# Kernel optimization log

Hardware: AMD Instinct MI355X
Metric: run time of the kernel (lower is better)

## Reference

```python
import jax, jax.numpy as jnp
import numpy as np

IN_F = 4096
OUT_F = 11008
GROUP = 128
NGROUPS = IN_F // GROUP
MAX_INT = 15  # 2**4 - 1


def setup_inputs() -> dict:
    key = jax.random.key(0)
    k1, k2, k3, k4, k5 = jax.random.split(key, 5)
    x = jax.random.normal(k1, (4, 2048, IN_F), dtype=jnp.float32)
    qweight = jax.random.randint(k2, (OUT_F, IN_F), 0, MAX_INT + 1, dtype=jnp.int32)
    scales = jax.random.uniform(k3, (OUT_F, NGROUPS), dtype=jnp.float32) * 0.01 + 1e-4
    zeros = jax.random.uniform(k4, (OUT_F, NGROUPS), dtype=jnp.float32) * MAX_INT
    b = jax.random.normal(k5, (OUT_F,), dtype=jnp.float32)
    return {"x": x, "qweight": qweight, "scales": scales, "zeros": zeros, "b": b}


def reference(x, qweight, scales, zeros, b):
    # Group-wise dequantization: W[o, i] = (q[o, i] - zeros[o, g(i)]) * scales[o, g(i)]
    s_rep = jnp.repeat(scales, GROUP, axis=1)  # [OUT_F, IN_F]
    z_rep = jnp.repeat(zeros, GROUP, axis=1)   # [OUT_F, IN_F]
    w_fp = (qweight.astype(x.dtype) - z_rep.astype(x.dtype)) * s_rep.astype(x.dtype)
    # F.linear: x @ W.T + b
    out = jnp.einsum('bsi,oi->bso', x, w_fp) + b.astype(x.dtype)
    return out
```

## Files before the change

### kernel.cpp

```cpp
#include <hip/hip_runtime.h>
#include <hip/hip_bf16.h>


#define K_DIM 4096
#define N_DIM 11008
#define M_DIM 8192
#define NGRP 32

typedef __bf16 bf16x8 __attribute__((ext_vector_type(8)));
typedef float f32x4 __attribute__((ext_vector_type(4)));
typedef unsigned short u16x8 __attribute__((ext_vector_type(8)));

__device__ __forceinline__ unsigned short f2bf(float f) {
  unsigned u = __builtin_bit_cast(unsigned, f);
  return (unsigned short)((u + 0x7FFFu + ((u >> 16) & 1u)) >> 16);
}

__device__ __forceinline__ void gload_lds16(const void* g, void* l) {
  __builtin_amdgcn_global_load_lds(
      (const __attribute__((address_space(1))) unsigned int*)(unsigned long long)g,
      (__attribute__((address_space(3))) unsigned int*)(unsigned int)(unsigned long long)l,
      16, 0, 0);
}

__global__ __launch_bounds__(256) void cvt_x_kernel(const float4* __restrict__ x4,
                                                    u16x8* __restrict__ xb) {
  int i = blockIdx.x * 256 + threadIdx.x;
  float4 a = x4[2 * i], b = x4[2 * i + 1];
  u16x8 r;
  r[0] = f2bf(a.x); r[1] = f2bf(a.y); r[2] = f2bf(a.z); r[3] = f2bf(a.w);
  r[4] = f2bf(b.x); r[5] = f2bf(b.y); r[6] = f2bf(b.z); r[7] = f2bf(b.w);
  xb[i] = r;
}

__global__ __launch_bounds__(256) void dequant_kernel(const int4* __restrict__ q4,
                                                      const float* __restrict__ scales,
                                                      const float* __restrict__ zeros,
                                                      u16x8* __restrict__ wb) {
  int t = blockIdx.x * 256 + threadIdx.x;
  int o = t >> 9;
  int j8 = t & 511;
  int g = j8 >> 4;
  float s = scales[o * NGRP + g];
  float z = zeros[o * NGRP + g];
  float nzs = -z * s;
  int4 qa = q4[2 * t], qb = q4[2 * t + 1];
  u16x8 r;
  r[0] = f2bf(fmaf((float)qa.x, s, nzs));
  r[1] = f2bf(fmaf((float)qa.y, s, nzs));
  r[2] = f2bf(fmaf((float)qa.z, s, nzs));
  r[3] = f2bf(fmaf((float)qa.w, s, nzs));
  r[4] = f2bf(fmaf((float)qb.x, s, nzs));
  r[5] = f2bf(fmaf((float)qb.y, s, nzs));
  r[6] = f2bf(fmaf((float)qb.z, s, nzs));
  r[7] = f2bf(fmaf((float)qb.w, s, nzs));
  wb[t] = r;
}

#define BAR() __builtin_amdgcn_s_barrier()
#define SCHED0() __builtin_amdgcn_sched_barrier(0)

__global__ __launch_bounds__(512, 2) void gemm_kernel(const unsigned short* __restrict__ A,
                                                      const unsigned short* __restrict__ B,
                                                      const float* __restrict__ bias,
                                                      float* __restrict__ C) {
  extern __shared__ unsigned short smem[];
  unsigned short* sAb = smem;
  unsigned short* sBb = smem + 32768;

  const int bid = blockIdx.x;
  const int swz = (bid & 7) * 172 + (bid >> 3);
  const int tm = swz / 43, tn = swz % 43;

  const int tid = threadIdx.x;
  const int w = tid >> 6, l = tid & 63;
  const int wr = w >> 2, wc = w & 3;

  const int dsto = w * 512 + l * 8;
  const int gs = (l & 7) ^ (l >> 3);
  const unsigned short* gA = A + (size_t)(tm * 256 + (tid >> 3)) * K_DIM + gs * 8;
  const unsigned short* gB = B + (size_t)(tn * 256 + (tid >> 3)) * K_DIM + gs * 8;

#define STG_A(tt, h, dst)                                                       \
  do {                                                                          \
    const unsigned short* _s = gA + (size_t)(h) * 128 * K_DIM + (tt) * 64;      \
    gload_lds16(_s, (dst) + dsto);                                              \
    gload_lds16(_s + 64 * K_DIM, (dst) + 4096 + dsto);                          \
  } while (0)
#define STG_B(tt, h, dst)                                                       \
  do {                                                                          \
    const unsigned short* _s = gB + (size_t)(h) * 128 * K_DIM + (tt) * 64;      \
    gload_lds16(_s, (dst) + dsto);                                              \
    gload_lds16(_s + 64 * K_DIM, (dst) + 4096 + dsto);                          \
  } while (0)

  const int fr = l & 15, sb = l >> 4, x7 = l & 7;
  const int abase = (wr * 64 + fr) * 64;
  const int bbase = (wc * 32 + fr) * 64;
  const int k0 = (sb ^ x7) * 8;
  const int k1 = ((sb + 4) ^ x7) * 8;

  bf16x8 av[4][2], bva[2][2], bvb[2][2];
  f32x4 acc[8][4] = {};

#define READ_A(half)                                                     \
  {                                                                      \
    _Pragma("unroll") for (int m = 0; m < 4; ++m) {                      \
      av[m][0] = *(const bf16x8*)((half) + abase + m * 1024 + k0);       \
      av[m][1] = *(const bf16x8*)((half) + abase + m * 1024 + k1);       \
    }                                                                    \
  }
#define READ_B(half, arr)                                                \
  {                                                                      \
    _Pragma("unroll") for (int n = 0; n < 2; ++n) {                      \
      arr[n][0] = *(const bf16x8*)((half) + bbase + n * 1024 + k0);      \
      arr[n][1] = *(const bf16x8*)((half) + bbase + n * 1024 + k1);      \
    }                                                                    \
  }
#define MFMA_Q(mh, nh, arr)                                                        \
  {                                                                                \
    __builtin_amdgcn_s_setprio(1);                                                 \
    _Pragma("unroll") for (int kk = 0; kk < 2; ++kk)                               \
    _Pragma("unroll") for (int m = 0; m < 4; ++m)                                  \
    _Pragma("unroll") for (int nn = 0; nn < 2; ++nn)                               \
      acc[(mh)*4 + m][(nh)*2 + nn] = __builtin_amdgcn_mfma_f32_16x16x32_bf16(      \
          av[m][kk], arr[nn][kk], acc[(mh)*4 + m][(nh)*2 + nn], 0, 0, 0);          \
    __builtin_amdgcn_s_setprio(0);                                                 \
  }

#define TILE(tnext, curA, curB, nxtA, nxtB, has_next)                    \
  {                                                                      \
    if (has_next) {                                                      \
      STG_A(tnext, 0, nxtA);                                             \
      STG_A(tnext, 1, (nxtA) + 8192);                                    \
      STG_B(tnext, 0, nxtB);                                             \
      STG_B(tnext, 1, (nxtB) + 8192);                                    \
    }                                                                    \
    READ_A(curA);                                                        \
    READ_B(curB, bva);                                                   \
    READ_B((curB) + 8192, bvb);                                          \
    MFMA_Q(0, 0, bva);                                                   \
    MFMA_Q(0, 1, bvb);                                                   \
    READ_A((curA) + 8192);                                               \
    MFMA_Q(1, 1, bvb);                                                   \
    MFMA_Q(1, 0, bva);                                                   \
    asm volatile("s_waitcnt vmcnt(0)" ::: "memory");                     \
    BAR();                                                               \
    SCHED0();                                                            \
  }

  STG_A(0, 0, sAb);
  STG_A(0, 1, sAb + 8192);
  STG_B(0, 0, sBb);
  STG_B(0, 1, sBb + 8192);
  asm volatile("s_waitcnt vmcnt(0)" ::: "memory");
  BAR();
  SCHED0();

  for (int tt = 0; tt < 32; ++tt) {
    TILE(2 * tt + 1, sAb, sBb, sAb + 16384, sBb + 16384, 1);
    TILE(2 * tt + 2, sAb + 16384, sBb + 16384, sAb, sBb, (tt < 31));
  }

  const int r0 = tm * 256 + wr * 64 + sb * 4;
  const int c0 = tn * 256 + wc * 32 + fr;
#pragma unroll
  for (int n = 0; n < 4; ++n) {
    const int col = c0 + (n >> 1) * 128 + (n & 1) * 16;
    const float bv = bias[col];
#pragma unroll
    for (int mi = 0; mi < 8; ++mi) {
      const int row = r0 + (mi >> 2) * 128 + (mi & 3) * 16;
#pragma unroll
      for (int jj = 0; jj < 4; ++jj)
        C[(size_t)(row + jj) * N_DIM + col] = acc[mi][n][jj] + bv;
    }
  }
}

extern "C" void kernel_launch(void* const* d_in, const int* in_sizes, int n_in,
                              void* d_out, int out_size, void* d_ws, size_t ws_size,
                              hipStream_t stream) {
  const float* x = (const float*)d_in[0];
  const int* qw = (const int*)d_in[1];
  const float* sc = (const float*)d_in[2];
  const float* zr = (const float*)d_in[3];
  const float* bs = (const float*)d_in[4];
  float* out = (float*)d_out;

  const size_t xb_bytes = (size_t)M_DIM * K_DIM * 2;
  const size_t wb_bytes = (size_t)N_DIM * K_DIM * 2;
  if (ws_size < xb_bytes + wb_bytes) return;

  unsigned short* xb = (unsigned short*)d_ws;
  unsigned short* wb = (unsigned short*)((char*)d_ws + xb_bytes);

  (void)hipFuncSetAttribute((const void*)gemm_kernel,
                            hipFuncAttributeMaxDynamicSharedMemorySize, 131072);

  cvt_x_kernel<<<(M_DIM * K_DIM / 8) / 256, 256, 0, stream>>>((const float4*)x, (u16x8*)xb);
  dequant_kernel<<<(N_DIM * K_DIM / 8) / 256, 256, 0, stream>>>((const int4*)qw, sc, zr,
                                                                (u16x8*)wb);
  gemm_kernel<<<(M_DIM / 256) * (N_DIM / 256), 512, 131072, stream>>>(xb, wb, bs, out);
}
```

Baseline: 751.6 us.

## Restructure GEMM LDS pipeline to read-then-stage and merge the prep kernels

The GEMM main loop now reads the whole A and B tiles from LDS into registers up front, using a second A register set. It then waits and synchronises, issues the global-to-LDS loads for tile t+2 into the buffer it just freed, and runs all MFMAs under raised priority. The prologue preloads two tiles, so global loads overlap a full tile of compute instead of being issued before the reads. The x conversion and weight dequant kernels are merged into one launch to drop a kernel boundary. In exchange, register pressure goes up, and the per-tile vmcnt(0) wait plus barrier still serialises part of the pipeline.

Measured after the change: 865.2 us. 1.15x slower.

```diff
diff --git a/kernel.cpp b/kernel.cpp
--- a/kernel.cpp
+++ b/kernel.cpp
@@ -23,38 +23,40 @@
       16, 0, 0);
 }
 
-__global__ __launch_bounds__(256) void cvt_x_kernel(const float4* __restrict__ x4,
-                                                    u16x8* __restrict__ xb) {
-  int i = blockIdx.x * 256 + threadIdx.x;
-  float4 a = x4[2 * i], b = x4[2 * i + 1];
-  u16x8 r;
-  r[0] = f2bf(a.x); r[1] = f2bf(a.y); r[2] = f2bf(a.z); r[3] = f2bf(a.w);
-  r[4] = f2bf(b.x); r[5] = f2bf(b.y); r[6] = f2bf(b.z); r[7] = f2bf(b.w);
-  xb[i] = r;
-}
-
-__global__ __launch_bounds__(256) void dequant_kernel(const int4* __restrict__ q4,
-                                                      const float* __restrict__ scales,
-                                                      const float* __restrict__ zeros,
-                                                      u16x8* __restrict__ wb) {
-  int t = blockIdx.x * 256 + threadIdx.x;
-  int o = t >> 9;
-  int j8 = t & 511;
-  int g = j8 >> 4;
-  float s = scales[o * NGRP + g];
-  float z = zeros[o * NGRP + g];
-  float nzs = -z * s;
-  int4 qa = q4[2 * t], qb = q4[2 * t + 1];
-  u16x8 r;
-  r[0] = f2bf(fmaf((float)qa.x, s, nzs));
-  r[1] = f2bf(fmaf((float)qa.y, s, nzs));
-  r[2] = f2bf(fmaf((float)qa.z, s, nzs));
-  r[3] = f2bf(fmaf((float)qa.w, s, nzs));
-  r[4] = f2bf(fmaf((float)qb.x, s, nzs));
-  r[5] = f2bf(fmaf((float)qb.y, s, nzs));
-  r[6] = f2bf(fmaf((float)qb.z, s, nzs));
-  r[7] = f2bf(fmaf((float)qb.w, s, nzs));
-  wb[t] = r;
+__global__ __launch_bounds__(256) void prep_kernel(const float4* __restrict__ x4,
+                                                   const int4* __restrict__ q4,
+                                                   const float* __restrict__ scales,
+                                                   const float* __restrict__ zeros,
+                                                   u16x8* __restrict__ xb,
+                                                   u16x8* __restrict__ wb) {
+  const int bid = blockIdx.x;
+  if (bid < 16384) {
+    int i = bid * 256 + threadIdx.x;
+    float4 a = x4[2 * i], b = x4[2 * i + 1];
+    u16x8 r;
+    r[0] = f2bf(a.x); r[1] = f2bf(a.y); r[2] = f2bf(a.z); r[3] = f2bf(a.w);
+    r[4] = f2bf(b.x); r[5] = f2bf(b.y); r[6] = f2bf(b.z); r[7] = f2bf(b.w);
+    xb[i] = r;
+  } else {
+    int t = (bid - 16384) * 256 + threadIdx.x;
+    int o = t >> 9;
+    int j8 = t & 511;
+    int g = j8 >> 4;
+    float s = scales[o * NGRP + g];
+    float z = zeros[o * NGRP + g];
+    float nzs = -z * s;
+    int4 qa = q4[2 * t], qb = q4[2 * t + 1];
+    u16x8 r;
+    r[0] = f2bf(fmaf((float)qa.x, s, nzs));
+    r[1] = f2bf(fmaf((float)qa.y, s, nzs));
+    r[2] = f2bf(fmaf((float)qa.z, s, nzs));
+    r[3] = f2bf(fmaf((float)qa.w, s, nzs));
+    r[4] = f2bf(fmaf((float)qb.x, s, nzs));
+    r[5] = f2bf(fmaf((float)qb.y, s, nzs));
+    r[6] = f2bf(fmaf((float)qb.z, s, nzs));
+    r[7] = f2bf(fmaf((float)qb.w, s, nzs));
+    wb[t] = r;
+  }
 }
 
 #define BAR() __builtin_amdgcn_s_barrier()
@@ -100,14 +102,14 @@
   const int k0 = (sb ^ x7) * 8;
   const int k1 = ((sb + 4) ^ x7) * 8;
 
-  bf16x8 av[4][2], bva[2][2], bvb[2][2];
+  bf16x8 av0[4][2], av1[4][2], bva[2][2], bvb[2][2];
   f32x4 acc[8][4] = {};
 
-#define READ_A(half)                                                     \
+#define READ_A(half, avv)                                                \
   {                                                                      \
     _Pragma("unroll") for (int m = 0; m < 4; ++m) {                      \
-      av[m][0] = *(const bf16x8*)((half) + abase + m * 1024 + k0);       \
-      av[m][1] = *(const bf16x8*)((half) + abase + m * 1024 + k1);       \
+      avv[m][0] = *(const bf16x8*)((half) + abase + m * 1024 + k0);      \
+      avv[m][1] = *(const bf16x8*)((half) + abase + m * 1024 + k1);      \
     }                                                                    \
   }
 #define READ_B(half, arr)                                                \
@@ -117,49 +119,54 @@
       arr[n][1] = *(const bf16x8*)((half) + bbase + n * 1024 + k1);      \
     }                                                                    \
   }
-#define MFMA_Q(mh, nh, arr)                                                        \
+#define MFMA_Q(mh, nh, arr, avv)                                                   \
   {                                                                                \
-    __builtin_amdgcn_s_setprio(1);                                                 \
     _Pragma("unroll") for (int kk = 0; kk < 2; ++kk)                               \
     _Pragma("unroll") for (int m = 0; m < 4; ++m)                                  \
     _Pragma("unroll") for (int nn = 0; nn < 2; ++nn)                               \
       acc[(mh)*4 + m][(nh)*2 + nn] = __builtin_amdgcn_mfma_f32_16x16x32_bf16(      \
-          av[m][kk], arr[nn][kk], acc[(mh)*4 + m][(nh)*2 + nn], 0, 0, 0);          \
-    __builtin_amdgcn_s_setprio(0);                                                 \
-  }
-
-#define TILE(tnext, curA, curB, nxtA, nxtB, has_next)                    \
+          avv[m][kk], arr[nn][kk], acc[(mh)*4 + m][(nh)*2 + nn], 0, 0, 0);         \
+  }
+
+#define TILE(tt, curA, curB, do_stage)                                   \
   {                                                                      \
-    if (has_next) {                                                      \
-      STG_A(tnext, 0, nxtA);                                             \
-      STG_A(tnext, 1, (nxtA) + 8192);                                    \
-      STG_B(tnext, 0, nxtB);                                             \
-      STG_B(tnext, 1, (nxtB) + 8192);                                    \
-    }                                                                    \
-    READ_A(curA);                                                        \
+    READ_A(curA, av0);                                                   \
+    READ_A((curA) + 8192, av1);                                          \
     READ_B(curB, bva);                                                   \
     READ_B((curB) + 8192, bvb);                                          \
-    MFMA_Q(0, 0, bva);                                                   \
-    MFMA_Q(0, 1, bvb);                                                   \
-    READ_A((curA) + 8192);                                               \
-    MFMA_Q(1, 1, bvb);                                                   \
-    MFMA_Q(1, 0, bva);                                                   \
-    asm volatile("s_waitcnt vmcnt(0)" ::: "memory");                     \
+    asm volatile("s_waitcnt vmcnt(0) lgkmcnt(0)" ::: "memory");          \
+    SCHED0();                                                            \
     BAR();                                                               \
     SCHED0();                                                            \
+    if (do_stage) {                                                      \
+      STG_A(tt + 2, 0, curA);                                            \
+      STG_A(tt + 2, 1, (curA) + 8192);                                   \
+      STG_B(tt + 2, 0, curB);                                            \
+      STG_B(tt + 2, 1, (curB) + 8192);                                   \
+    }                                                                    \
+    __builtin_amdgcn_s_setprio(1);                                       \
+    MFMA_Q(0, 0, bva, av0);                                              \
+    MFMA_Q(0, 1, bvb, av0);                                              \
+    MFMA_Q(1, 1, bvb, av1);                                              \
+    MFMA_Q(1, 0, bva, av1);                                              \
+    __builtin_amdgcn_s_setprio(0);                                       \
   }
 
   STG_A(0, 0, sAb);
   STG_A(0, 1, sAb + 8192);
   STG_B(0, 0, sBb);
   STG_B(0, 1, sBb + 8192);
-  asm volatile("s_waitcnt vmcnt(0)" ::: "memory");
+  STG_A(1, 0, sAb + 16384);
+  STG_A(1, 1, sAb + 16384 + 8192);
+  STG_B(1, 0, sBb + 16384);
+  STG_B(1, 1, sBb + 16384 + 8192);
+  asm volatile("s_waitcnt vmcnt(8)" ::: "memory");
   BAR();
   SCHED0();
 
   for (int tt = 0; tt < 32; ++tt) {
-    TILE(2 * tt + 1, sAb, sBb, sAb + 16384, sBb + 16384, 1);
-    TILE(2 * tt + 2, sAb + 16384, sBb + 16384, sAb, sBb, (tt < 31));
+    TILE(2 * tt, sAb, sBb, (tt < 31));
+    TILE(2 * tt + 1, sAb + 16384, sBb + 16384, (tt < 31));
   }
 
   const int r0 = tm * 256 + wr * 64 + sb * 4;
@@ -198,8 +205,7 @@
   (void)hipFuncSetAttribute((const void*)gemm_kernel,
                             hipFuncAttributeMaxDynamicSharedMemorySize, 131072);
 
-  cvt_x_kernel<<<(M_DIM * K_DIM / 8) / 256, 256, 0, stream>>>((const float4*)x, (u16x8*)xb);
-  dequant_kernel<<<(N_DIM * K_DIM / 8) / 256, 256, 0, stream>>>((const int4*)qw, sc, zr,
-                                                                (u16x8*)wb);
+  prep_kernel<<<16384 + 22016, 256, 0, stream>>>((const float4*)x, (const int4*)qw, sc, zr,
+                                                 (u16x8*)xb, (u16x8*)wb);
   gemm_kernel<<<(M_DIM / 256) * (N_DIM / 256), 512, 131072, stream>>>(xb, wb, bs, out);
 }
```
